# Optimization experiments

Hardware: AMD Instinct MI355X
Metric: run time of the kernel (lower is better)

## Reference

```python
import jax, jax.numpy as jnp
import numpy as np

B = 8192
INPUT_DIM = 1024
PATH_DIM = 256
HIDDEN_DIM = 1024
OUTPUT_DIM = 1024
STEPS = 50


def setup_inputs() -> dict:
    key = jax.random.key(0)
    ks = jax.random.split(key, 12)
    s = lambda fan_in: 1.0 / np.sqrt(fan_in)
    x0 = jax.random.normal(ks[0], (B, INPUT_DIM), dtype=jnp.float32)
    W_pe = jax.random.uniform(ks[1], (INPUT_DIM, PATH_DIM), jnp.float32, -s(INPUT_DIM), s(INPUT_DIM))
    b_pe = jax.random.uniform(ks[2], (PATH_DIM,), jnp.float32, -s(INPUT_DIM), s(INPUT_DIM))
    W_hi = jax.random.uniform(ks[3], (INPUT_DIM, HIDDEN_DIM), jnp.float32, -s(INPUT_DIM), s(INPUT_DIM))
    b_hi = jax.random.uniform(ks[4], (HIDDEN_DIM,), jnp.float32, -s(INPUT_DIM), s(INPUT_DIM))
    f_in = HIDDEN_DIM + PATH_DIM
    W1 = jax.random.uniform(ks[5], (f_in, HIDDEN_DIM), jnp.float32, -s(f_in), s(f_in))
    b1 = jax.random.uniform(ks[6], (HIDDEN_DIM,), jnp.float32, -s(f_in), s(f_in))
    W2 = jax.random.uniform(ks[7], (HIDDEN_DIM, HIDDEN_DIM), jnp.float32, -s(HIDDEN_DIM), s(HIDDEN_DIM))
    b2 = jax.random.uniform(ks[8], (HIDDEN_DIM,), jnp.float32, -s(HIDDEN_DIM), s(HIDDEN_DIM))
    W_ro = jax.random.uniform(ks[9], (HIDDEN_DIM, OUTPUT_DIM), jnp.float32, -s(HIDDEN_DIM), s(HIDDEN_DIM))
    b_ro = jax.random.uniform(ks[10], (OUTPUT_DIM,), jnp.float32, -s(HIDDEN_DIM), s(HIDDEN_DIM))
    return {"x0": x0, "W_pe": W_pe, "b_pe": b_pe, "W_hi": W_hi, "b_hi": b_hi,
            "W1": W1, "b1": b1, "W2": W2, "b2": b2, "W_ro": W_ro, "b_ro": b_ro}


def reference(x0, W_pe, b_pe, W_hi, b_hi, W1, b1, W2, b2, W_ro, b_ro):
    dt = 1.0 / float(STEPS)
    g = x0 @ W_pe + b_pe          # [B, path_dim]
    z0 = x0 @ W_hi + b_hi          # [B, hidden_dim]
    ts = dt * jnp.arange(1, STEPS + 1, dtype=jnp.float32)  # t after each step

    def step(z, t):
        u_t = t * g                                  # [B, path_dim]
        inp = jnp.concatenate([z, u_t], axis=-1)     # [B, hidden+path]
        dz = jnp.tanh(inp @ W1 + b1) @ W2 + b2       # [B, hidden_dim]
        return z + dt * dz, None

    z, _ = jax.lax.scan(step, z0, ts)
    return z @ W_ro + b_ro
```

## Files before the change

kernel.cpp:

```cpp
#include <hip/hip_runtime.h>
#include <hip/hip_bf16.h>

typedef __hip_bfloat16 bf16;
typedef __bf16 bf16x8 __attribute__((ext_vector_type(8)));
typedef float f32x4 __attribute__((ext_vector_type(4)));

#define ROWS   32
#define HID    1024
#define PATH   256
#define NSTEP  50
#define P      1032
#define SMEM_BYTES (2 * ROWS * P * 2)

__device__ __forceinline__ f32x4 mfma16(bf16x8 a, bf16x8 b, f32x4 c) {
    return __builtin_amdgcn_mfma_f32_16x16x32_bf16(a, b, c, 0, 0, 0);
}

__device__ __forceinline__ float tanh_fast(float x) {
    float e = __expf(2.0f * x);
    return 1.0f - 2.0f / (e + 1.0f);
}

__device__ __forceinline__ bf16x8 ldcvt8(const float* __restrict__ p) {
    f32x4 lo = *(const f32x4*)p;
    f32x4 hi = *(const f32x4*)(p + 4);
    bf16x8 r;
    #pragma unroll
    for (int j = 0; j < 4; j++) { r[j] = (__bf16)lo[j]; r[4 + j] = (__bf16)hi[j]; }
    return r;
}

__device__ __forceinline__ unsigned bfbits(float f) {
    __hip_bfloat16 h = __float2bfloat16(f);
    unsigned short u; __builtin_memcpy(&u, &h, 2);
    return (unsigned)u;
}
__device__ __forceinline__ unsigned bfpack2(float lo, float hi) {
    return bfbits(lo) | (bfbits(hi) << 16);
}
__device__ __forceinline__ float bflo(unsigned u) { return __uint_as_float(u << 16); }
__device__ __forceinline__ float bfhi(unsigned u) { return __uint_as_float(u & 0xffff0000u); }

__global__ void pack_frag(const float* __restrict__ src, bf16* __restrict__ dst, int N) {
    int kb = blockIdx.x, nb = blockIdx.y, l = threadIdx.x;
    int lm = l & 15, lq = l >> 4;
    bf16x8 v;
    #pragma unroll
    for (int j = 0; j < 8; j++)
        v[j] = __float2bfloat16(src[(size_t)(kb * 32 + lq * 8 + j) * N + nb * 16 + lm]);
    *(bf16x8*)(dst + ((size_t)(kb * gridDim.y + nb) * 64 + l) * 8) = v;
}

template<int KB>
__device__ __forceinline__ void gemm4p(const bf16* __restrict__ lds,
                                       const bf16* __restrict__ Wp,
                                       int wave, int lane, int rot, f32x4 (&acc)[2][4]) {
    static_assert((KB & (KB - 1)) == 0, "KB must be a power of two");
    const int lm = lane & 15, lq = lane >> 4;
    const bf16* a0b = lds + lm * P + lq * 8;
    const bf16* a1b = a0b + 16 * P;
    const int woff = wave * 2048 + lane * 8;

    bf16x8 w[4], a0A, a1A, a0B, a1B;
    {
        const int k0 = rot & (KB - 1);
        const int k1 = (rot + 1) & (KB - 1);
        const bf16* wp = Wp + (size_t)k0 * 32768 + woff;
        #pragma unroll
        for (int nt = 0; nt < 4; nt++) w[nt] = *(const bf16x8*)(wp + nt * 512);
        a0A = *(const bf16x8*)(a0b + k0 * 32);
        a1A = *(const bf16x8*)(a1b + k0 * 32);
        a0B = *(const bf16x8*)(a0b + k1 * 32);
        a1B = *(const bf16x8*)(a1b + k1 * 32);
    }
    #pragma unroll 2
    for (int kb = 0; kb < KB; kb += 2) {
        const int kw1 = (kb + 1 + rot) & (KB - 1);
        const int ka1 = (kb + 2 + rot) & (KB - 1);
        const bf16* wp1 = Wp + (size_t)kw1 * 32768 + woff;
        acc[0][0] = mfma16(a0A, w[0], acc[0][0]);
        acc[1][0] = mfma16(a1A, w[0], acc[1][0]);
        w[0] = *(const bf16x8*)(wp1);
        acc[0][1] = mfma16(a0A, w[1], acc[0][1]);
        acc[1][1] = mfma16(a1A, w[1], acc[1][1]);
        w[1] = *(const bf16x8*)(wp1 + 512);
        acc[0][2] = mfma16(a0A, w[2], acc[0][2]);
        acc[1][2] = mfma16(a1A, w[2], acc[1][2]);
        w[2] = *(const bf16x8*)(wp1 + 1024);
        acc[0][3] = mfma16(a0A, w[3], acc[0][3]);
        acc[1][3] = mfma16(a1A, w[3], acc[1][3]);
        w[3] = *(const bf16x8*)(wp1 + 1536);
        a0A = *(const bf16x8*)(a0b + ka1 * 32);
        a1A = *(const bf16x8*)(a1b + ka1 * 32);
        const int kw2 = ka1;
        const int ka2 = (kb + 3 + rot) & (KB - 1);
        const bf16* wp2 = Wp + (size_t)kw2 * 32768 + woff;
        acc[0][0] = mfma16(a0B, w[0], acc[0][0]);
        acc[1][0] = mfma16(a1B, w[0], acc[1][0]);
        w[0] = *(const bf16x8*)(wp2);
        acc[0][1] = mfma16(a0B, w[1], acc[0][1]);
        acc[1][1] = mfma16(a1B, w[1], acc[1][1]);
        w[1] = *(const bf16x8*)(wp2 + 512);
        acc[0][2] = mfma16(a0B, w[2], acc[0][2]);
        acc[1][2] = mfma16(a1B, w[2], acc[1][2]);
        w[2] = *(const bf16x8*)(wp2 + 1024);
        acc[0][3] = mfma16(a0B, w[3], acc[0][3]);
        acc[1][3] = mfma16(a1B, w[3], acc[1][3]);
        w[3] = *(const bf16x8*)(wp2 + 1536);
        a0B = *(const bf16x8*)(a0b + ka2 * 32);
        a1B = *(const bf16x8*)(a1b + ka2 * 32);
    }
}

__global__ __launch_bounds__(1024, 4) void cde_main(
    const float* __restrict__ x0,  const float* __restrict__ b_pe, const float* __restrict__ b_hi,
    const float* __restrict__ b1v, const float* __restrict__ b2v,  const float* __restrict__ b_ro,
    const bf16* __restrict__ WpeP, const bf16* __restrict__ WhiP,
    const bf16* __restrict__ W1zP, const bf16* __restrict__ W1uP,
    const bf16* __restrict__ W2P,  const bf16* __restrict__ WroP,
    float* __restrict__ out)
{
    extern __shared__ bf16 smem[];
    bf16* inp = smem;
    bf16* th  = smem + ROWS * P;

    const int tid  = threadIdx.x;
    const int wave = tid >> 6;
    const int lane = tid & 63;
    const int lm   = lane & 15;
    const int lq   = lane >> 4;
    const int rot  = (blockIdx.x >> 3) & 31;
    const long row0 = (long)blockIdx.x * ROWS;

    f32x4 z[2][4];
    f32x4 g[2];
    uint2 cu_pk[2][4];

    #pragma unroll
    for (int nt = 0; nt < 4; nt++) {
        float b = b_hi[wave * 64 + nt * 16 + lm];
        #pragma unroll
        for (int r = 0; r < 4; r++) { z[0][nt][r] = b; z[1][nt][r] = b; }
    }
    {
        float b = b_pe[wave * 16 + lm];
        #pragma unroll
        for (int r = 0; r < 4; r++) { g[0][r] = b; g[1][r] = b; }
    }
    for (int kb = 0; kb < HID / 32; kb++) {
        int kbr = kb + rot; if (kbr >= 32) kbr -= 32;
        bf16x8 a0 = ldcvt8(x0 + (row0 +      lm) * HID + kbr * 32 + lq * 8);
        bf16x8 a1 = ldcvt8(x0 + (row0 + 16 + lm) * HID + kbr * 32 + lq * 8);
        const bf16* wp = WhiP + (((size_t)kbr * 64 + wave * 4) * 64 + lane) * 8;
        #pragma unroll
        for (int nt = 0; nt < 4; nt++) {
            bf16x8 bb = *(const bf16x8*)(wp + nt * 512);
            z[0][nt] = mfma16(a0, bb, z[0][nt]);
            z[1][nt] = mfma16(a1, bb, z[1][nt]);
        }
        bf16x8 pb = *(const bf16x8*)(WpeP + (((size_t)kbr * 16 + wave) * 64 + lane) * 8);
        g[0] = mfma16(a0, pb, g[0]);
        g[1] = mfma16(a1, pb, g[1]);
    }

    #pragma unroll
    for (int mt = 0; mt < 2; mt++)
        #pragma unroll
        for (int r = 0; r < 4; r++)
            inp[(mt * 16 + lq * 4 + r) * P + wave * 16 + lm] = __float2bfloat16(g[mt][r]);
    __syncthreads();
    {
        f32x4 cu[2][4];
        #pragma unroll
        for (int mt = 0; mt < 2; mt++)
            #pragma unroll
            for (int nt = 0; nt < 4; nt++)
                #pragma unroll
                for (int r = 0; r < 4; r++) cu[mt][nt][r] = 0.0f;
        for (int kb = 0; kb < PATH / 32; kb++) {
            const bf16* wp = W1uP + (((size_t)kb * 64 + wave * 4) * 64 + lane) * 8;
            bf16x8 a0 = *(const bf16x8*)(inp + lm * P + kb * 32 + lq * 8);
            bf16x8 a1 = *(const bf16x8*)(inp + (16 + lm) * P + kb * 32 + lq * 8);
            #pragma unroll
            for (int nt = 0; nt < 4; nt++) {
                bf16x8 bb = *(const bf16x8*)(wp + nt * 512);
                cu[0][nt] = mfma16(a0, bb, cu[0][nt]);
                cu[1][nt] = mfma16(a1, bb, cu[1][nt]);
            }
        }
        #pragma unroll
        for (int mt = 0; mt < 2; mt++)
            #pragma unroll
            for (int nt = 0; nt < 4; nt++)
                cu_pk[mt][nt] = make_uint2(bfpack2(cu[mt][nt][0], cu[mt][nt][1]),
                                           bfpack2(cu[mt][nt][2], cu[mt][nt][3]));
    }
    __syncthreads();

    const float DT = 1.0f / (float)NSTEP;

    unsigned b12[4];
    #pragma unroll
    for (int nt = 0; nt < 4; nt++)
        b12[nt] = bfpack2(b1v[wave * 64 + nt * 16 + lm],
                          DT * b2v[wave * 64 + nt * 16 + lm]);

    for (int s = 0; s < NSTEP; s++) {
        float t = DT * (float)(s + 1);

        #pragma unroll
        for (int mt = 0; mt < 2; mt++)
            #pragma unroll
            for (int nt = 0; nt < 4; nt++)
                #pragma unroll
                for (int r = 0; r < 4; r++)
                    inp[(mt * 16 + lq * 4 + r) * P + wave * 64 + nt * 16 + lm] =
                        __float2bfloat16(z[mt][nt][r]);
        __syncthreads();

        {
            f32x4 acc[2][4];
            #pragma unroll
            for (int mt = 0; mt < 2; mt++)
                #pragma unroll
                for (int nt = 0; nt < 4; nt++) {
                    float b1 = bflo(b12[nt]);
                    unsigned px = cu_pk[mt][nt].x, py = cu_pk[mt][nt].y;
                    acc[mt][nt][0] = fmaf(t, bflo(px), b1);
                    acc[mt][nt][1] = fmaf(t, bfhi(px), b1);
                    acc[mt][nt][2] = fmaf(t, bflo(py), b1);
                    acc[mt][nt][3] = fmaf(t, bfhi(py), b1);
                }
            gemm4p<HID / 32>(inp, W1zP, wave, lane, rot, acc);
            #pragma unroll
            for (int mt = 0; mt < 2; mt++)
                #pragma unroll
                for (int nt = 0; nt < 4; nt++)
                    #pragma unroll
                    for (int r = 0; r < 4; r++)
                        th[(mt * 16 + lq * 4 + r) * P + wave * 64 + nt * 16 + lm] =
                            __float2bfloat16(DT * tanh_fast(acc[mt][nt][r]));
        }
        __syncthreads();

        {
            #pragma unroll
            for (int mt = 0; mt < 2; mt++)
                #pragma unroll
                for (int nt = 0; nt < 4; nt++) {
                    float db = bfhi(b12[nt]);
                    #pragma unroll
                    for (int r = 0; r < 4; r++) z[mt][nt][r] += db;
                }
            gemm4p<HID / 32>(th, W2P, wave, lane, rot, z);
        }
    }

    #pragma unroll
    for (int mt = 0; mt < 2; mt++)
        #pragma unroll
        for (int nt = 0; nt < 4; nt++)
            #pragma unroll
            for (int r = 0; r < 4; r++)
                inp[(mt * 16 + lq * 4 + r) * P + wave * 64 + nt * 16 + lm] =
                    __float2bfloat16(z[mt][nt][r]);
    __syncthreads();
    {
        f32x4 acc[2][4];
        #pragma unroll
        for (int nt = 0; nt < 4; nt++) {
            float b = b_ro[wave * 64 + nt * 16 + lm];
            #pragma unroll
            for (int r = 0; r < 4; r++) { acc[0][nt][r] = b; acc[1][nt][r] = b; }
        }
        gemm4p<HID / 32>(inp, WroP, wave, lane, rot, acc);
        #pragma unroll
        for (int mt = 0; mt < 2; mt++)
            #pragma unroll
            for (int nt = 0; nt < 4; nt++)
                #pragma unroll
                for (int r = 0; r < 4; r++)
                    out[(row0 + mt * 16 + lq * 4 + r) * HID + wave * 64 + nt * 16 + lm] =
                        acc[mt][nt][r];
    }
}

extern "C" void kernel_launch(void* const* d_in, const int* in_sizes, int n_in,
                              void* d_out, int out_size, void* d_ws, size_t ws_size,
                              hipStream_t stream) {
    (void)in_sizes; (void)n_in; (void)out_size; (void)ws_size;
    const float* x0  = (const float*)d_in[0];
    const float* Wpe = (const float*)d_in[1];
    const float* bpe = (const float*)d_in[2];
    const float* Whi = (const float*)d_in[3];
    const float* bhi = (const float*)d_in[4];
    const float* W1  = (const float*)d_in[5];
    const float* b1  = (const float*)d_in[6];
    const float* W2  = (const float*)d_in[7];
    const float* b2  = (const float*)d_in[8];
    const float* Wro = (const float*)d_in[9];
    const float* bro = (const float*)d_in[10];

    bf16* ws   = (bf16*)d_ws;
    bf16* WpeP = ws;
    bf16* WhiP = WpeP + 256 * 1024;
    bf16* W1zP = WhiP + 1024 * 1024;
    bf16* W1uP = W1zP + 1024 * 1024;
    bf16* W2P  = W1uP + 256 * 1024;
    bf16* WroP = W2P  + 1024 * 1024;

    hipLaunchKernelGGL(pack_frag, dim3(1024 / 32, 256 / 16), dim3(64), 0, stream, Wpe, WpeP, 256);
    hipLaunchKernelGGL(pack_frag, dim3(1024 / 32, 1024 / 16), dim3(64), 0, stream, Whi, WhiP, 1024);
    hipLaunchKernelGGL(pack_frag, dim3(1024 / 32, 1024 / 16), dim3(64), 0, stream, W1, W1zP, 1024);
    hipLaunchKernelGGL(pack_frag, dim3(256 / 32, 1024 / 16), dim3(64), 0, stream,
                       W1 + (size_t)1024 * 1024, W1uP, 1024);
    hipLaunchKernelGGL(pack_frag, dim3(1024 / 32, 1024 / 16), dim3(64), 0, stream, W2, W2P, 1024);
    hipLaunchKernelGGL(pack_frag, dim3(1024 / 32, 1024 / 16), dim3(64), 0, stream, Wro, WroP, 1024);

    hipFuncSetAttribute((const void*)cde_main,
                        hipFuncAttributeMaxDynamicSharedMemorySize, SMEM_BYTES);
    hipLaunchKernelGGL(cde_main, dim3(8192 / ROWS), dim3(1024), SMEM_BYTES, stream,
                       x0, bpe, bhi, b1, b2, bro, WpeP, WhiP, W1zP, W1uP, W2P, WroP,
                       (float*)d_out);
}
```

Before: 2.631 ms.

## Prefetch next GEMM's first weight tile across barriers and peel last iteration

Moves the first weight-fragment load of each GEMM out of the GEMM and issues it right after the previous GEMM finishes, so global-load latency overlaps the tanh epilogue, LDS stores and barriers. The K loop is peeled so its final iteration does not issue wasted loads, and unrolling is set to 1. The k-rotation per block changes from a blockIdx>>3-based value to (blockIdx&7)*4, which changes how concurrent blocks stagger their weight accesses. The prefetch costs extra live registers, and the unroll-1 loop may add loop overhead.

```diff
diff --git a/kernel.cpp b/kernel.cpp
--- a/kernel.cpp
+++ b/kernel.cpp
@@ -51,33 +51,38 @@
     *(bf16x8*)(dst + ((size_t)(kb * gridDim.y + nb) * 64 + l) * 8) = v;
 }
 
+__device__ __forceinline__ void loadw4(const bf16* __restrict__ Wp, int k, int woff,
+                                       bf16x8 (&w)[4]) {
+    const bf16* wp = Wp + (size_t)k * 32768 + woff;
+    #pragma unroll
+    for (int nt = 0; nt < 4; nt++) w[nt] = *(const bf16x8*)(wp + nt * 512);
+}
+
 template<int KB>
-__device__ __forceinline__ void gemm4p(const bf16* __restrict__ lds,
+__device__ __forceinline__ void gemm4h(const bf16* __restrict__ lds,
                                        const bf16* __restrict__ Wp,
-                                       int wave, int lane, int rot, f32x4 (&acc)[2][4]) {
+                                       int wave, int lane, int rot,
+                                       bf16x8 (&w)[4], f32x4 (&acc)[2][4]) {
     static_assert((KB & (KB - 1)) == 0, "KB must be a power of two");
     const int lm = lane & 15, lq = lane >> 4;
     const bf16* a0b = lds + lm * P + lq * 8;
     const bf16* a1b = a0b + 16 * P;
     const int woff = wave * 2048 + lane * 8;
 
-    bf16x8 w[4], a0A, a1A, a0B, a1B;
-    {
-        const int k0 = rot & (KB - 1);
-        const int k1 = (rot + 1) & (KB - 1);
-        const bf16* wp = Wp + (size_t)k0 * 32768 + woff;
-        #pragma unroll
-        for (int nt = 0; nt < 4; nt++) w[nt] = *(const bf16x8*)(wp + nt * 512);
-        a0A = *(const bf16x8*)(a0b + k0 * 32);
-        a1A = *(const bf16x8*)(a1b + k0 * 32);
-        a0B = *(const bf16x8*)(a0b + k1 * 32);
-        a1B = *(const bf16x8*)(a1b + k1 * 32);
-    }
-    #pragma unroll 2
-    for (int kb = 0; kb < KB; kb += 2) {
+    const int k0 = rot & (KB - 1);
+    const int k1 = (rot + 1) & (KB - 1);
+    bf16x8 a0A = *(const bf16x8*)(a0b + k0 * 32);
+    bf16x8 a1A = *(const bf16x8*)(a1b + k0 * 32);
+    bf16x8 a0B = *(const bf16x8*)(a0b + k1 * 32);
+    bf16x8 a1B = *(const bf16x8*)(a1b + k1 * 32);
+
+    #pragma unroll 1
+    for (int kb = 0; kb < KB - 2; kb += 2) {
         const int kw1 = (kb + 1 + rot) & (KB - 1);
-        const int ka1 = (kb + 2 + rot) & (KB - 1);
+        const int kw2 = (kb + 2 + rot) & (KB - 1);
+        const int kw3 = (kb + 3 + rot) & (KB - 1);
         const bf16* wp1 = Wp + (size_t)kw1 * 32768 + woff;
+        const bf16* wp2 = Wp + (size_t)kw2 * 32768 + woff;
         acc[0][0] = mfma16(a0A, w[0], acc[0][0]);
         acc[1][0] = mfma16(a1A, w[0], acc[1][0]);
         w[0] = *(const bf16x8*)(wp1);
@@ -90,11 +95,8 @@
         acc[0][3] = mfma16(a0A, w[3], acc[0][3]);
         acc[1][3] = mfma16(a1A, w[3], acc[1][3]);
         w[3] = *(const bf16x8*)(wp1 + 1536);
-        a0A = *(const bf16x8*)(a0b + ka1 * 32);
-        a1A = *(const bf16x8*)(a1b + ka1 * 32);
-        const int kw2 = ka1;
-        const int ka2 = (kb + 3 + rot) & (KB - 1);
-        const bf16* wp2 = Wp + (size_t)kw2 * 32768 + woff;
+        a0A = *(const bf16x8*)(a0b + kw2 * 32);
+        a1A = *(const bf16x8*)(a1b + kw2 * 32);
         acc[0][0] = mfma16(a0B, w[0], acc[0][0]);
         acc[1][0] = mfma16(a1B, w[0], acc[1][0]);
         w[0] = *(const bf16x8*)(wp2);
@@ -107,8 +109,32 @@
         acc[0][3] = mfma16(a0B, w[3], acc[0][3]);
         acc[1][3] = mfma16(a1B, w[3], acc[1][3]);
         w[3] = *(const bf16x8*)(wp2 + 1536);
-        a0B = *(const bf16x8*)(a0b + ka2 * 32);
-        a1B = *(const bf16x8*)(a1b + ka2 * 32);
+        a0B = *(const bf16x8*)(a0b + kw3 * 32);
+        a1B = *(const bf16x8*)(a1b + kw3 * 32);
+    }
+    {
+        const int kwl = (KB - 1 + rot) & (KB - 1);
+        const bf16* wpl = Wp + (size_t)kwl * 32768 + woff;
+        acc[0][0] = mfma16(a0A, w[0], acc[0][0]);
+        acc[1][0] = mfma16(a1A, w[0], acc[1][0]);
+        w[0] = *(const bf16x8*)(wpl);
+        acc[0][1] = mfma16(a0A, w[1], acc[0][1]);
+        acc[1][1] = mfma16(a1A, w[1], acc[1][1]);
+        w[1] = *(const bf16x8*)(wpl + 512);
+        acc[0][2] = mfma16(a0A, w[2], acc[0][2]);
+        acc[1][2] = mfma16(a1A, w[2], acc[1][2]);
+        w[2] = *(const bf16x8*)(wpl + 1024);
+        acc[0][3] = mfma16(a0A, w[3], acc[0][3]);
+        acc[1][3] = mfma16(a1A, w[3], acc[1][3]);
+        w[3] = *(const bf16x8*)(wpl + 1536);
+        acc[0][0] = mfma16(a0B, w[0], acc[0][0]);
+        acc[1][0] = mfma16(a1B, w[0], acc[1][0]);
+        acc[0][1] = mfma16(a0B, w[1], acc[0][1]);
+        acc[1][1] = mfma16(a1B, w[1], acc[1][1]);
+        acc[0][2] = mfma16(a0B, w[2], acc[0][2]);
+        acc[1][2] = mfma16(a1B, w[2], acc[1][2]);
+        acc[0][3] = mfma16(a0B, w[3], acc[0][3]);
+        acc[1][3] = mfma16(a1B, w[3], acc[1][3]);
     }
 }
 
@@ -129,7 +155,8 @@
     const int lane = tid & 63;
     const int lm   = lane & 15;
     const int lq   = lane >> 4;
-    const int rot  = (blockIdx.x >> 3) & 31;
+    const int rot  = (blockIdx.x & 7) * 4;
+    const int woff = wave * 2048 + lane * 8;
     const long row0 = (long)blockIdx.x * ROWS;
 
     f32x4 z[2][4];
@@ -204,6 +231,9 @@
     for (int nt = 0; nt < 4; nt++)
         b12[nt] = bfpack2(b1v[wave * 64 + nt * 16 + lm],
                           DT * b2v[wave * 64 + nt * 16 + lm]);
+
+    bf16x8 wpre[4];
+    loadw4(W1zP, rot, woff, wpre);
 
     for (int s = 0; s < NSTEP; s++) {
         float t = DT * (float)(s + 1);
@@ -231,7 +261,8 @@
                     acc[mt][nt][2] = fmaf(t, bflo(py), b1);
                     acc[mt][nt][3] = fmaf(t, bfhi(py), b1);
                 }
-            gemm4p<HID / 32>(inp, W1zP, wave, lane, rot, acc);
+            gemm4h<HID / 32>(inp, W1zP, wave, lane, rot, wpre, acc);
+            loadw4(W2P, rot, woff, wpre);
             #pragma unroll
             for (int mt = 0; mt < 2; mt++)
                 #pragma unroll
@@ -252,7 +283,9 @@
                     #pragma unroll
                     for (int r = 0; r < 4; r++) z[mt][nt][r] += db;
                 }
-            gemm4p<HID / 32>(th, W2P, wave, lane, rot, z);
+            gemm4h<HID / 32>(th, W2P, wave, lane, rot, wpre, z);
+            const bf16* nW = (s + 1 < NSTEP) ? W1zP : WroP;
+            loadw4(nW, rot, woff, wpre);
         }
     }
 
@@ -273,7 +306,7 @@
             #pragma unroll
             for (int r = 0; r < 4; r++) { acc[0][nt][r] = b; acc[1][nt][r] = b; }
         }
-        gemm4p<HID / 32>(inp, WroP, wave, lane, rot, acc);
+        gemm4h<HID / 32>(inp, WroP, wave, lane, rot, wpre, acc);
         #pragma unroll
         for (int mt = 0; mt < 2; mt++)
             #pragma unroll
```

Result: slower. 2.688 ms (+2.2%).

## Prefetch next GEMM's first weight tile across phases and stagger k-rotation per wave

Applied to the files above, without the earlier changes.

Replaces the GEMM inner routine with a double-buffered version that takes its first weight fragment already loaded from the previous phase, so each GEMM's initial global load overlaps the tanh epilogue, the LDS stores and the barrier. It also offsets each wave's starting k-block so waves in a block read different LDS columns and weight tiles at the same moment, and reorders the MFMA/load interleave with unroll 1. The cost is extra live registers for the prefetched weights, which may pressure occupancy at 1024 threads per block.

```diff
diff --git a/kernel.cpp b/kernel.cpp
--- a/kernel.cpp
+++ b/kernel.cpp
@@ -51,64 +51,70 @@
     *(bf16x8*)(dst + ((size_t)(kb * gridDim.y + nb) * 64 + l) * 8) = v;
 }
 
+__device__ __forceinline__ void loadw4(const bf16* __restrict__ Wp, int k, int woff,
+                                       bf16x8 (&w)[4]) {
+    const bf16* wp = Wp + (size_t)k * 32768 + woff;
+    #pragma unroll
+    for (int nt = 0; nt < 4; nt++) w[nt] = *(const bf16x8*)(wp + nt * 512);
+}
+
 template<int KB>
-__device__ __forceinline__ void gemm4p(const bf16* __restrict__ lds,
+__device__ __forceinline__ void gemm4d(const bf16* __restrict__ lds,
                                        const bf16* __restrict__ Wp,
-                                       int wave, int lane, int rot, f32x4 (&acc)[2][4]) {
+                                       int wave, int lane, int krot,
+                                       bf16x8 (&wA)[4], f32x4 (&acc)[2][4]) {
     static_assert((KB & (KB - 1)) == 0, "KB must be a power of two");
     const int lm = lane & 15, lq = lane >> 4;
     const bf16* a0b = lds + lm * P + lq * 8;
     const bf16* a1b = a0b + 16 * P;
     const int woff = wave * 2048 + lane * 8;
 
-    bf16x8 w[4], a0A, a1A, a0B, a1B;
+    bf16x8 wB[4];
     {
-        const int k0 = rot & (KB - 1);
-        const int k1 = (rot + 1) & (KB - 1);
-        const bf16* wp = Wp + (size_t)k0 * 32768 + woff;
-        #pragma unroll
-        for (int nt = 0; nt < 4; nt++) w[nt] = *(const bf16x8*)(wp + nt * 512);
-        a0A = *(const bf16x8*)(a0b + k0 * 32);
-        a1A = *(const bf16x8*)(a1b + k0 * 32);
-        a0B = *(const bf16x8*)(a0b + k1 * 32);
-        a1B = *(const bf16x8*)(a1b + k1 * 32);
-    }
-    #pragma unroll 2
+        const int k1 = (krot + 1) & (KB - 1);
+        const bf16* wp = Wp + (size_t)k1 * 32768 + woff;
+        #pragma unroll
+        for (int nt = 0; nt < 4; nt++) wB[nt] = *(const bf16x8*)(wp + nt * 512);
+    }
+    const int k0 = krot & (KB - 1);
+    bf16x8 a0 = *(const bf16x8*)(a0b + k0 * 32);
+    bf16x8 a1 = *(const bf16x8*)(a1b + k0 * 32);
+
+    #pragma unroll 1
     for (int kb = 0; kb < KB; kb += 2) {
-        const int kw1 = (kb + 1 + rot) & (KB - 1);
-        const int ka1 = (kb + 2 + rot) & (KB - 1);
-        const bf16* wp1 = Wp + (size_t)kw1 * 32768 + woff;
-        acc[0][0] = mfma16(a0A, w[0], acc[0][0]);
-        acc[1][0] = mfma16(a1A, w[0], acc[1][0]);
-        w[0] = *(const bf16x8*)(wp1);
-        acc[0][1] = mfma16(a0A, w[1], acc[0][1]);
-        acc[1][1] = mfma16(a1A, w[1], acc[1][1]);
-        w[1] = *(const bf16x8*)(wp1 + 512);
-        acc[0][2] = mfma16(a0A, w[2], acc[0][2]);
-        acc[1][2] = mfma16(a1A, w[2], acc[1][2]);
-        w[2] = *(const bf16x8*)(wp1 + 1024);
-        acc[0][3] = mfma16(a0A, w[3], acc[0][3]);
-        acc[1][3] = mfma16(a1A, w[3], acc[1][3]);
-        w[3] = *(const bf16x8*)(wp1 + 1536);
-        a0A = *(const bf16x8*)(a0b + ka1 * 32);
-        a1A = *(const bf16x8*)(a1b + ka1 * 32);
-        const int kw2 = ka1;
-        const int ka2 = (kb + 3 + rot) & (KB - 1);
+        const int ka1 = (kb + 1 + krot) & (KB - 1);
+        const int kw2 = (kb + 2 + krot) & (KB - 1);
+        const int kw3 = (kb + 3 + krot) & (KB - 1);
         const bf16* wp2 = Wp + (size_t)kw2 * 32768 + woff;
-        acc[0][0] = mfma16(a0B, w[0], acc[0][0]);
-        acc[1][0] = mfma16(a1B, w[0], acc[1][0]);
-        w[0] = *(const bf16x8*)(wp2);
-        acc[0][1] = mfma16(a0B, w[1], acc[0][1]);
-        acc[1][1] = mfma16(a1B, w[1], acc[1][1]);
-        w[1] = *(const bf16x8*)(wp2 + 512);
-        acc[0][2] = mfma16(a0B, w[2], acc[0][2]);
-        acc[1][2] = mfma16(a1B, w[2], acc[1][2]);
-        w[2] = *(const bf16x8*)(wp2 + 1024);
-        acc[0][3] = mfma16(a0B, w[3], acc[0][3]);
-        acc[1][3] = mfma16(a1B, w[3], acc[1][3]);
-        w[3] = *(const bf16x8*)(wp2 + 1536);
-        a0B = *(const bf16x8*)(a0b + ka2 * 32);
-        a1B = *(const bf16x8*)(a1b + ka2 * 32);
+        const bf16* wp3 = Wp + (size_t)kw3 * 32768 + woff;
+        acc[0][0] = mfma16(a0, wA[0], acc[0][0]);
+        acc[0][1] = mfma16(a0, wA[1], acc[0][1]);
+        acc[0][2] = mfma16(a0, wA[2], acc[0][2]);
+        acc[0][3] = mfma16(a0, wA[3], acc[0][3]);
+        a0 = *(const bf16x8*)(a0b + ka1 * 32);
+        acc[1][0] = mfma16(a1, wA[0], acc[1][0]);
+        wA[0] = *(const bf16x8*)(wp2);
+        acc[1][1] = mfma16(a1, wA[1], acc[1][1]);
+        wA[1] = *(const bf16x8*)(wp2 + 512);
+        acc[1][2] = mfma16(a1, wA[2], acc[1][2]);
+        wA[2] = *(const bf16x8*)(wp2 + 1024);
+        acc[1][3] = mfma16(a1, wA[3], acc[1][3]);
+        wA[3] = *(const bf16x8*)(wp2 + 1536);
+        a1 = *(const bf16x8*)(a1b + ka1 * 32);
+        acc[0][0] = mfma16(a0, wB[0], acc[0][0]);
+        acc[0][1] = mfma16(a0, wB[1], acc[0][1]);
+        acc[0][2] = mfma16(a0, wB[2], acc[0][2]);
+        acc[0][3] = mfma16(a0, wB[3], acc[0][3]);
+        a0 = *(const bf16x8*)(a0b + kw2 * 32);
+        acc[1][0] = mfma16(a1, wB[0], acc[1][0]);
+        wB[0] = *(const bf16x8*)(wp3);
+        acc[1][1] = mfma16(a1, wB[1], acc[1][1]);
+        wB[1] = *(const bf16x8*)(wp3 + 512);
+        acc[1][2] = mfma16(a1, wB[2], acc[1][2]);
+        wB[2] = *(const bf16x8*)(wp3 + 1024);
+        acc[1][3] = mfma16(a1, wB[3], acc[1][3]);
+        wB[3] = *(const bf16x8*)(wp3 + 1536);
+        a1 = *(const bf16x8*)(a1b + kw2 * 32);
     }
 }
 
@@ -130,6 +136,8 @@
     const int lm   = lane & 15;
     const int lq   = lane >> 4;
     const int rot  = (blockIdx.x >> 3) & 31;
+    const int krot = (rot + wave * 2) & 31;
+    const int woff = wave * 2048 + lane * 8;
     const long row0 = (long)blockIdx.x * ROWS;
 
     f32x4 z[2][4];
@@ -148,7 +156,7 @@
         for (int r = 0; r < 4; r++) { g[0][r] = b; g[1][r] = b; }
     }
     for (int kb = 0; kb < HID / 32; kb++) {
-        int kbr = kb + rot; if (kbr >= 32) kbr -= 32;
+        int kbr = kb + krot; if (kbr >= 32) kbr -= 32;
         bf16x8 a0 = ldcvt8(x0 + (row0 +      lm) * HID + kbr * 32 + lq * 8);
         bf16x8 a1 = ldcvt8(x0 + (row0 + 16 + lm) * HID + kbr * 32 + lq * 8);
         const bf16* wp = WhiP + (((size_t)kbr * 64 + wave * 4) * 64 + lane) * 8;
@@ -204,6 +212,9 @@
     for (int nt = 0; nt < 4; nt++)
         b12[nt] = bfpack2(b1v[wave * 64 + nt * 16 + lm],
                           DT * b2v[wave * 64 + nt * 16 + lm]);
+
+    bf16x8 wpre[4];
+    loadw4(W1zP, krot, woff, wpre);
 
     for (int s = 0; s < NSTEP; s++) {
         float t = DT * (float)(s + 1);
@@ -231,7 +242,8 @@
                     acc[mt][nt][2] = fmaf(t, bflo(py), b1);
                     acc[mt][nt][3] = fmaf(t, bfhi(py), b1);
                 }
-            gemm4p<HID / 32>(inp, W1zP, wave, lane, rot, acc);
+            gemm4d<HID / 32>(inp, W1zP, wave, lane, krot, wpre, acc);
+            loadw4(W2P, krot, woff, wpre);
             #pragma unroll
             for (int mt = 0; mt < 2; mt++)
                 #pragma unroll
@@ -252,7 +264,9 @@
                     #pragma unroll
                     for (int r = 0; r < 4; r++) z[mt][nt][r] += db;
                 }
-            gemm4p<HID / 32>(th, W2P, wave, lane, rot, z);
+            gemm4d<HID / 32>(th, W2P, wave, lane, krot, wpre, z);
+            const bf16* nW = (s + 1 < NSTEP) ? W1zP : WroP;
+            loadw4(nW, krot, woff, wpre);
         }
     }
 
@@ -273,7 +287,7 @@
             #pragma unroll
             for (int r = 0; r < 4; r++) { acc[0][nt][r] = b; acc[1][nt][r] = b; }
         }
-        gemm4p<HID / 32>(inp, WroP, wave, lane, rot, acc);
+        gemm4d<HID / 32>(inp, WroP, wave, lane, krot, wpre, acc);
         #pragma unroll
         for (int mt = 0; mt < 2; mt++)
             #pragma unroll
```

New measurement: 2.943 ms. 1.12x slower.
